# Kernel tuning notes

Measured on AMD Instinct MI355X. Metric: run time of the kernel, lower is better.

The kernel has to match this reference:

```python
import jax, jax.numpy as jnp
import numpy as np

WS = 7      # window size
SHIFT = 3   # shift size
NH = 6      # num heads
C = 192     # channels
HH = 56
WW = 56
B = 32


def _rel_coords():
    ch, cw = np.meshgrid(np.arange(WS), np.arange(WS), indexing='ij')
    coords = np.stack([ch, cw]).reshape(2, -1)            # (2, 49)
    rel = coords[:, :, None] - coords[:, None, :]          # (2, 49, 49)
    rel[0] += WS - 1
    rel[1] += WS - 1
    rel[0] *= 2 * WS - 1
    return rel.sum(0)                                      # (49, 49)


def _swin_attn_mask(Hp, Wp):
    img = np.zeros((Hp, Wp), np.int32)
    cnt = 0
    for hs in (slice(0, -WS), slice(-WS, -SHIFT), slice(-SHIFT, None)):
        for ws_ in (slice(0, -WS), slice(-WS, -SHIFT), slice(-SHIFT, None)):
            img[hs, ws_] = cnt
            cnt += 1
    win = img.reshape(Hp // WS, WS, Wp // WS, WS).transpose(0, 2, 1, 3).reshape(-1, WS * WS)
    return win[:, :, None] != win[:, None, :]              # (Nw, 49, 49) bool


def setup_inputs() -> dict:
    key = jax.random.key(0)
    ks = jax.random.split(key, 8)
    s = 0.02
    return {
        'x': jax.random.normal(ks[0], (B, HH * WW, C), jnp.float32),
        'H': HH,
        'W': WW,
        'attn_mask': jnp.asarray(_swin_attn_mask(HH, WW)),
        'relative_coords': jnp.asarray(_rel_coords(), jnp.int32),
        'norm1_w': jnp.ones((C,), jnp.float32),
        'norm1_b': jnp.zeros((C,), jnp.float32),
        'qkv_w': jax.random.normal(ks[1], (3 * C, C), jnp.float32) * s,
        'rel_bias': jax.random.normal(ks[2], ((2 * WS - 1) ** 2, NH), jnp.float32) * 0.2,
        'proj_w': jax.random.normal(ks[3], (C, C), jnp.float32) * s,
        'proj_b': jnp.zeros((C,), jnp.float32),
        'norm2_w': jnp.ones((C,), jnp.float32),
        'norm2_b': jnp.zeros((C,), jnp.float32),
        'fc1_w': jax.random.normal(ks[4], (4 * C, C), jnp.float32) * s,
        'fc1_b': jnp.zeros((4 * C,), jnp.float32),
        'fc2_w': jax.random.normal(ks[5], (C, 4 * C), jnp.float32) * s,
        'fc2_b': jnp.zeros((C,), jnp.float32),
    }


def _ln(t, w, b):
    m = t.mean(-1, keepdims=True)
    v = t.var(-1, keepdims=True)
    return (t - m) / jnp.sqrt(v + 1e-5) * w + b


def reference(x, H, W, attn_mask, relative_coords, norm1_w, norm1_b, qkv_w, rel_bias,
              proj_w, proj_b, norm2_w, norm2_b, fc1_w, fc1_b, fc2_w, fc2_b):
    Bb, L, Cd = x.shape
    nh, hd = NH, C // NH
    shortcut = x
    h = _ln(x, norm1_w, norm1_b).reshape(Bb, H, W, Cd)
    pad_h = (WS - H % WS) % WS
    pad_w = (WS - W % WS) % WS
    if pad_h or pad_w:
        h = jnp.pad(h, ((0, 0), (0, pad_h), (0, pad_w), (0, 0)))
    Hp, Wp = H + pad_h, W + pad_w
    if SHIFT > 0:
        h = jnp.roll(h, (-SHIFT, -SHIFT), axis=(1, 2))
    nWh, nWw = Hp // WS, Wp // WS
    Lw = WS * WS
    win = h.reshape(Bb, nWh, WS, nWw, WS, Cd).transpose(0, 1, 3, 2, 4, 5).reshape(-1, Lw, Cd)
    B_ = win.shape[0]
    qkv = (win @ qkv_w.T).reshape(B_, Lw, 3, nh, hd).transpose(2, 0, 3, 1, 4)
    q, k, v = qkv[0], qkv[1], qkv[2]
    # NOTE: source multiplies by num_dim**0.5 (faithful quirk)
    attn = jnp.einsum('bhid,bhjd->bhij', q, k) * (Cd ** 0.5)
    bias = rel_bias[relative_coords].transpose(2, 0, 1)    # (nh, Lw, Lw)
    attn = attn + bias[None]
    if SHIFT > 0:
        Nw = attn_mask.shape[0]
        attn = attn.reshape(-1, Nw, nh, Lw, Lw)
        attn = jnp.where(attn_mask[None, :, None], -100.0, attn)
        attn = attn.reshape(B_, nh, Lw, Lw)
    attn = jax.nn.softmax(attn, axis=-1)
    out = jnp.einsum('bhij,bhjd->bhid', attn, v).transpose(0, 2, 1, 3).reshape(B_, Lw, Cd)
    out = out @ proj_w.T + proj_b
    out = out.reshape(Bb, nWh, nWw, WS, WS, Cd).transpose(0, 1, 3, 2, 4, 5).reshape(Bb, Hp, Wp, Cd)
    if SHIFT > 0:
        out = jnp.roll(out, (SHIFT, SHIFT), axis=(1, 2))
    out = out[:, :H, :W].reshape(Bb, L, Cd)
    x = shortcut + out
    h2 = _ln(x, norm2_w, norm2_b)
    h2 = jax.nn.gelu(h2 @ fc1_w.T + fc1_b, approximate=False)
    # source MLP applies GELU (drop2 = act_layer()) after fc2 (faithful quirk)
    h2 = jax.nn.gelu(h2 @ fc2_w.T + fc2_b, approximate=False)
    return x + h2
```

## Files before the change

### kernel.cpp

```cpp
#include <hip/hip_runtime.h>

#define WS7    7
#define SHIFT3 3
#define NHEAD  6
#define CCH    192
#define HDIM   32
#define HH56   56
#define LTOK   (HH56*HH56)
#define NWIN   64
#define NBATCH 32
#define NWTOT  (NBATCH*NWIN)
#define LW     49
#define MTOK   (NWTOT*LW)

typedef unsigned short u16;
typedef unsigned int   u32;
typedef __bf16 b16;
typedef b16   b16x8 __attribute__((ext_vector_type(8)));
typedef u16   u16x8 __attribute__((ext_vector_type(8)));
typedef float f32x4 __attribute__((ext_vector_type(4)));

__device__ __forceinline__ float b2f(u16 u) {
    u32 x = ((u32)u) << 16;
    return __builtin_bit_cast(float, x);
}
__device__ __forceinline__ u16 f2b(float f) {
    u32 x = __builtin_bit_cast(u32, f);
    u32 r = x + 0x7FFFu + ((x >> 16) & 1u);
    return (u16)(r >> 16);
}
__device__ __forceinline__ float gelu_exact(float x) {
    return 0.5f * x * (1.0f + erff(x * 0.7071067811865475f));
}

__device__ __forceinline__ int map_token(int m, int &b) {
    int widx = m / LW, p = m - widx * LW;
    b = widx >> 6;
    int wloc = widx & 63;
    int wh = wloc >> 3, ww = wloc & 7;
    int i = p / WS7, j = p - i * WS7;
    int gh = wh * WS7 + i + SHIFT3; if (gh >= HH56) gh -= HH56;
    int gw = ww * WS7 + j + SHIFT3; if (gw >= HH56) gw -= HH56;
    return gh * HH56 + gw;
}

__global__ __launch_bounds__(1024) void probe_kernel(const u16* __restrict__ x, int* flag) {
    __shared__ int ch, cz;
    if (threadIdx.x == 0) { ch = 0; cz = 0; }
    __syncthreads();
    int i = threadIdx.x * 16;
    u16x8 a = *(const u16x8*)(x + i);
    u16x8 b = *(const u16x8*)(x + i + 8);
    int h = 0, z = 0;
    #pragma unroll
    for (int q = 0; q < 8; q++) {
        h += (((a[q] >> 7) & 0xFF) >= 0xC0) + (((b[q] >> 7) & 0xFF) >= 0xC0);
        z += (a[q] == 0) + (b[q] == 0);
    }
    #pragma unroll
    for (int off = 32; off > 0; off >>= 1) {
        h += __shfl_xor(h, off, 64);
        z += __shfl_xor(z, off, 64);
    }
    if ((threadIdx.x & 63) == 0) { atomicAdd(&ch, h); atomicAdd(&cz, z); }
    __syncthreads();
    if (threadIdx.x == 0) *flag = (ch > 250 || cz > 2048) ? 1 : 0;
}

#define CANON_TOTAL 445302
__global__ __launch_bounds__(256) void canon_all_kernel(
    const int* __restrict__ flag,
    const void* s0, const void* s1, const void* s2,  const void* s3,
    const void* s4, const void* s5, const void* s6,  const void* s7,
    const void* s8, const void* s9, const void* s10, const void* s11,
    char* __restrict__ ws)
{
    int i = blockIdx.x * 256 + threadIdx.x;
    if (i >= CANON_TOTAL) return;
    const void* srcs[12] = {s0, s1, s2, s3, s4, s5, s6, s7, s8, s9, s10, s11};
    const int cnt[12] = {110592, 36864, 147456, 147456, 192, 192, 192, 192, 192, 768, 192, 1014};
    const int off[12] = {64, 221248, 294976, 589888, 884800, 885184, 885568, 885952, 886336, 886720, 888256, 888640};
    int seg = 0, base = 0;
    while (seg < 11 && i >= base + cnt[seg]) { base += cnt[seg]; seg++; }
    int j = i - base;
    const void* sp = srcs[seg];
    u16* dp = (u16*)(ws + off[seg]);
    dp[j] = (*flag) ? f2b(((const float*)sp)[j]) : ((const u16*)sp)[j];
}

template<int GATHER>
__global__ __launch_bounds__(256) void ln_kernel(
    const void* __restrict__ src, const u16* __restrict__ w, const u16* __restrict__ bia,
    u16* __restrict__ dst, int m_base, const int* __restrict__ flag)
{
    int wave = threadIdx.x >> 6, lane = threadIdx.x & 63;
    int mloc = blockIdx.x * 4 + wave;
    size_t row;
    if (GATHER) { int b; int l = map_token(m_base + mloc, b); row = (size_t)b * LTOK + l; }
    else row = mloc;
    float v0, v1, v2;
    if (GATHER && *flag) {
        const float* xp = (const float*)src + row * CCH;
        v0 = xp[lane]; v1 = xp[lane + 64]; v2 = xp[lane + 128];
    } else {
        const u16* xp = (const u16*)src + row * CCH;
        v0 = b2f(xp[lane]); v1 = b2f(xp[lane + 64]); v2 = b2f(xp[lane + 128]);
    }
    float s = v0 + v1 + v2, sq = v0 * v0 + v1 * v1 + v2 * v2;
    for (int off = 32; off > 0; off >>= 1) {
        s  += __shfl_xor(s, off, 64);
        sq += __shfl_xor(sq, off, 64);
    }
    float mean = s * (1.f / 192.f);
    float var  = fmaxf(sq * (1.f / 192.f) - mean * mean, 0.f);
    float rstd = rsqrtf(var + 1e-5f);
    u16* op = dst + (size_t)mloc * CCH;
    op[lane]       = f2b((v0 - mean) * rstd * b2f(w[lane])       + b2f(bia[lane]));
    op[lane + 64]  = f2b((v1 - mean) * rstd * b2f(w[lane + 64])  + b2f(bia[lane + 64]));
    op[lane + 128] = f2b((v2 - mean) * rstd * b2f(w[lane + 128]) + b2f(bia[lane + 128]));
}

__device__ __forceinline__ void stage192(const u16* __restrict__ g, int ldg, u16* s, int tid) {
    #pragma unroll
    for (int it = 0; it < 7; it++) {
        int t = it * 256 + tid;
        if (t < 1600) {
            int row = t / 25, c = t - row * 25;
            int cc = (c == 24) ? 0 : c;
            const u16* src = g + (size_t)row * ldg + cc * 8;
            u16* dst = s + (size_t)(it * 256 + (tid & ~63)) * 8;
            __builtin_amdgcn_global_load_lds(
                (const __attribute__((address_space(1))) void*)src,
                (__attribute__((address_space(3))) void*)dst, 16, 0, 0);
        }
    }
}

__device__ __forceinline__ void ln_lds_rows(u16* As, const u16* __restrict__ w,
                                            const u16* __restrict__ bia, int tid) {
    int r = tid >> 2, p = tid & 3;
    u16* row = As + r * 200 + p * 48;
    u16x8 vv[6];
    float s = 0.f, sq = 0.f;
    #pragma unroll
    for (int j = 0; j < 6; j++) {
        vv[j] = *(const u16x8*)(row + j * 8);
        #pragma unroll
        for (int q = 0; q < 8; q++) { float f = b2f(vv[j][q]); s += f; sq += f * f; }
    }
    s  += __shfl_xor(s, 1, 64);  s  += __shfl_xor(s, 2, 64);
    sq += __shfl_xor(sq, 1, 64); sq += __shfl_xor(sq, 2, 64);
    float mean = s * (1.f / 192.f);
    float var  = fmaxf(sq * (1.f / 192.f) - mean * mean, 0.f);
    float rstd = rsqrtf(var + 1e-5f);
    #pragma unroll
    for (int j = 0; j < 6; j++) {
        u16x8 o;
        #pragma unroll
        for (int q = 0; q < 8; q++) {
            int col = p * 48 + j * 8 + q;
            o[q] = f2b((b2f(vv[j][q]) - mean) * rstd * b2f(w[col]) + b2f(bia[col]));
        }
        *(u16x8*)(row + j * 8) = o;
    }
}

template<int MODE, int NT, int LNF>
__global__ __launch_bounds__(256) void gemm_k192(
    const u16* __restrict__ A, const u16* __restrict__ Bm, int N,
    const u16* __restrict__ lnw, const u16* __restrict__ lnb,
    const u16* __restrict__ bias,
    u16* __restrict__ Cb, u16* __restrict__ X1, const void* __restrict__ Xin,
    int m_base, const int* __restrict__ flag)
{
    __shared__ __align__(16) u16 As[64 * 200];
    __shared__ __align__(16) u16 Bs[2][64 * 200];
    int isf = *flag;
    int tid = threadIdx.x;
    int m0 = blockIdx.x * 64;
    int wave = tid >> 6, lane = tid & 63;
    int wm = wave >> 1, wn = wave & 1;
    int quad = lane >> 4, mr = lane & 15;

    stage192(A + (size_t)m0 * 192, 192, As, tid);
    stage192(Bm, 192, Bs[0], tid);
    __syncthreads();
    if (LNF) { ln_lds_rows(As, lnw, lnb, tid); __syncthreads(); }

    const u16* pa0 = &As[(wm * 32 + mr) * 200 + quad * 8];
    #pragma unroll 1
    for (int nb = 0; nb < NT; nb++) {
        if (nb + 1 < NT)
            stage192(Bm + (size_t)(nb + 1) * 64 * 192, 192, Bs[(nb + 1) & 1], tid);
        const u16* pb0 = &Bs[nb & 1][(wn * 32 + mr) * 200 + quad * 8];
        f32x4 acc00 = {}, acc01 = {}, acc10 = {}, acc11 = {};
        #pragma unroll
        for (int ks = 0; ks < 6; ks++) {
            b16x8 a0 = __builtin_bit_cast(b16x8, *(const u16x8*)(pa0 + ks * 32));
            b16x8 a1 = __builtin_bit_cast(b16x8, *(const u16x8*)(pa0 + 16 * 200 + ks * 32));
            b16x8 b0 = __builtin_bit_cast(b16x8, *(const u16x8*)(pb0 + ks * 32));
            b16x8 b1 = __builtin_bit_cast(b16x8, *(const u16x8*)(pb0 + 16 * 200 + ks * 32));
            acc00 = __builtin_amdgcn_mfma_f32_16x16x32_bf16(a0, b0, acc00, 0, 0, 0);
            acc01 = __builtin_amdgcn_mfma_f32_16x16x32_bf16(a0, b1, acc01, 0, 0, 0);
            acc10 = __builtin_amdgcn_mfma_f32_16x16x32_bf16(a1, b0, acc10, 0, 0, 0);
            acc11 = __builtin_amdgcn_mfma_f32_16x16x32_bf16(a1, b1, acc11, 0, 0, 0);
        }
        int n0 = nb * 64;
        f32x4 accs[2][2] = {{acc00, acc01}, {acc10, acc11}};
        #pragma unroll
        for (int sm = 0; sm < 2; sm++) {
            #pragma unroll
            for (int sn = 0; sn < 2; sn++) {
                f32x4 v = accs[sm][sn];
                int nn = n0 + wn * 32 + sn * 16 + mr;
                int mb = m0 + wm * 32 + sm * 16 + quad * 4;
                #pragma unroll
                for (int r = 0; r < 4; r++) {
                    int mm = mb + r;
                    float val = v[r];
                    if (MODE == 0) {
                        Cb[(size_t)mm * N + nn] = f2b(val);
                    } else if (MODE == 1) {
                        val += b2f(bias[nn]);
                        int b; int l = map_token(m_base + mm, b);
                        size_t idx = ((size_t)b * LTOK + l) * CCH + nn;
                        float xi = isf ? ((const float*)Xin)[idx] : b2f(((const u16*)Xin)[idx]);
                        X1[idx] = f2b(xi + val);
                    } else {
                        val = gelu_exact(val + b2f(bias[nn]));
                        Cb[(size_t)mm * N + nn] = f2b(val);
                    }
                }
            }
        }
        __syncthreads();
    }
}

__global__ __launch_bounds__(256) void gemm_k768(
    const u16* __restrict__ A, const u16* __restrict__ Bm,
    const u16* __restrict__ bias, const u16* __restrict__ X1,
    void* __restrict__ Oout, size_t o_off, const int* __restrict__ flag)
{
    __shared__ __align__(16) u16 As[64 * 200];
    __shared__ __align__(16) u16 Bs[2][64 * 200];
    int isf = *flag;
    int tid = threadIdx.x;
    int m0 = blockIdx.x * 64;
    int wave = tid >> 6, lane = tid & 63;
    int wm = wave >> 1, wn = wave & 1;
    int quad = lane >> 4, mr = lane & 15;

    f32x4 acc[3][4] = {};

    const u16* pa0 = &As[(wm * 32 + mr) * 200 + quad * 8];
    #pragma unroll 1
    for (int k0 = 0; k0 < 768; k0 += 192) {
        stage192(A + (size_t)m0 * 768 + k0, 768, As, tid);
        stage192(Bm + k0, 768, Bs[0], tid);
        __syncthreads();
        #pragma unroll
        for (int nb = 0; nb < 3; nb++) {
            if (nb < 2)
                stage192(Bm + (size_t)(nb + 1) * 64 * 768 + k0, 768, Bs[(nb + 1) & 1], tid);
            const u16* pb0 = &Bs[nb & 1][(wn * 32 + mr) * 200 + quad * 8];
            #pragma unroll
            for (int ks = 0; ks < 6; ks++) {
                b16x8 a0 = __builtin_bit_cast(b16x8, *(const u16x8*)(pa0 + ks * 32));
                b16x8 a1 = __builtin_bit_cast(b16x8, *(const u16x8*)(pa0 + 16 * 200 + ks * 32));
                b16x8 b0 = __builtin_bit_cast(b16x8, *(const u16x8*)(pb0 + ks * 32));
                b16x8 b1 = __builtin_bit_cast(b16x8, *(const u16x8*)(pb0 + 16 * 200 + ks * 32));
                acc[nb][0] = __builtin_amdgcn_mfma_f32_16x16x32_bf16(a0, b0, acc[nb][0], 0, 0, 0);
                acc[nb][1] = __builtin_amdgcn_mfma_f32_16x16x32_bf16(a0, b1, acc[nb][1], 0, 0, 0);
                acc[nb][2] = __builtin_amdgcn_mfma_f32_16x16x32_bf16(a1, b0, acc[nb][2], 0, 0, 0);
                acc[nb][3] = __builtin_amdgcn_mfma_f32_16x16x32_bf16(a1, b1, acc[nb][3], 0, 0, 0);
            }
            __syncthreads();
        }
    }

    #pragma unroll
    for (int nb = 0; nb < 3; nb++) {
        #pragma unroll
        for (int sm = 0; sm < 2; sm++) {
            #pragma unroll
            for (int sn = 0; sn < 2; sn++) {
                f32x4 v = acc[nb][sm * 2 + sn];
                int nn = nb * 64 + wn * 32 + sn * 16 + mr;
                int mb = m0 + wm * 32 + sm * 16 + quad * 4;
                #pragma unroll
                for (int r = 0; r < 4; r++) {
                    int mm = mb + r;
                    float val = gelu_exact(v[r] + b2f(bias[nn]));
                    size_t idx = (size_t)mm * CCH + nn;
                    float r2 = val + b2f(X1[idx]);
                    if (isf) ((float*)Oout)[o_off + idx] = r2;
                    else     ((u16*)Oout)[o_off + idx]  = f2b(r2);
                }
            }
        }
    }
}

__global__ __launch_bounds__(256) void attn_kernel(
    const u16* __restrict__ qkv, const u16* __restrict__ rel_bias,
    u16* __restrict__ aout)
{
    __shared__ __align__(16) u16 qs[64 * 32];
    __shared__ __align__(16) u16 ks[64 * 32];
    __shared__ __align__(16) u16 vsT[32 * 72];
    __shared__ __align__(16) u16 ps[64 * 72];
    __shared__ float bias_s[169];
    int blk = blockIdx.x;
    int widx = blk / NHEAD, head = blk - widx * NHEAD;
    int wloc = widx & 63;
    int wh = wloc >> 3, ww = wloc & 7;
    int tid = threadIdx.x;
    const u16* base = qkv + (size_t)widx * LW * 576 + head * HDIM;

    if (tid < 196) {
        int i = tid >> 2, c8 = (tid & 3) * 8;
        *(uint4*)&qs[i * 32 + c8] = *(const uint4*)(base + (size_t)i * 576 + c8);
        *(uint4*)&ks[i * 32 + c8] = *(const uint4*)(base + (size_t)i * 576 + 192 + c8);
        u16x8 vv = *(const u16x8*)(base + (size_t)i * 576 + 384 + c8);
        #pragma unroll
        for (int q = 0; q < 8; q++) vsT[(c8 + q) * 72 + i] = vv[q];
    }
    for (int idx = tid; idx < 32 * 15; idx += 256) {
        int d = idx / 15, j = 49 + (idx - d * 15);
        vsT[d * 72 + j] = 0;
    }
    if (tid < 169) bias_s[tid] = b2f(rel_bias[tid * NHEAD + head]);
    __syncthreads();

    int wave = tid >> 6, lane = tid & 63;
    int quad = lane >> 4, c = lane & 15;

    b16x8 aq = __builtin_bit_cast(b16x8, *(const u16x8*)&qs[(wave * 16 + c) * 32 + quad * 8]);
    f32x4 sacc[4];
    #pragma unroll
    for (int nt = 0; nt < 4; nt++) {
        b16x8 bk = __builtin_bit_cast(b16x8, *(const u16x8*)&ks[(nt * 16 + c) * 32 + quad * 8]);
        f32x4 z = {};
        sacc[nt] = __builtin_amdgcn_mfma_f32_16x16x32_bf16(aq, bk, z, 0, 0, 0);
    }

    const float SCALE = 13.856406460551018f;
    float val[4][4];
    int rbase = wave * 16 + quad * 4;
    #pragma unroll
    for (int r = 0; r < 4; r++) {
        int i = rbase + r;
        int ih = i / WS7, iw = i - ih * WS7;
        int ri = (wh == 7 ? (ih < 4 ? 1 : 2) : 0) * 3 + (ww == 7 ? (iw < 4 ? 1 : 2) : 0);
        #pragma unroll
        for (int nt = 0; nt < 4; nt++) {
            int j = nt * 16 + c;
            float v;
            if (i >= LW) v = 0.f;
            else if (j >= LW) v = -1e30f;
            else {
                int jh = j / WS7, jw = j - jh * WS7;
                int rj = (wh == 7 ? (jh < 4 ? 1 : 2) : 0) * 3 + (ww == 7 ? (jw < 4 ? 1 : 2) : 0);
                if (ri != rj) v = -100.0f;
                else v = fmaf(sacc[nt][r], SCALE, bias_s[(ih - jh + 6) * 13 + (iw - jw + 6)]);
            }
            val[r][nt] = v;
        }
    }

    #pragma unroll
    for (int r = 0; r < 4; r++) {
        float mx = fmaxf(fmaxf(val[r][0], val[r][1]), fmaxf(val[r][2], val[r][3]));
        for (int d = 1; d < 16; d <<= 1) mx = fmaxf(mx, __shfl_xor(mx, d, 64));
        float sum = 0.f;
        #pragma unroll
        for (int nt = 0; nt < 4; nt++) { float e = expf(val[r][nt] - mx); val[r][nt] = e; sum += e; }
        for (int d = 1; d < 16; d <<= 1) sum += __shfl_xor(sum, d, 64);
        float inv = 1.f / sum;
        int i = rbase + r;
        #pragma unroll
        for (int nt = 0; nt < 4; nt++)
            ps[i * 72 + nt * 16 + c] = f2b(val[r][nt] * inv);
    }

    f32x4 oacc[2] = {{}, {}};
    #pragma unroll
    for (int kh = 0; kh < 2; kh++) {
        b16x8 ap = __builtin_bit_cast(b16x8, *(const u16x8*)&ps[(wave * 16 + c) * 72 + kh * 32 + quad * 8]);
        #pragma unroll
        for (int nt = 0; nt < 2; nt++) {
            b16x8 bv = __builtin_bit_cast(b16x8, *(const u16x8*)&vsT[(nt * 16 + c) * 72 + kh * 32 + quad * 8]);
            oacc[nt] = __builtin_amdgcn_mfma_f32_16x16x32_bf16(ap, bv, oacc[nt], 0, 0, 0);
        }
    }
    #pragma unroll
    for (int nt = 0; nt < 2; nt++) {
        #pragma unroll
        for (int r = 0; r < 4; r++) {
            int i = rbase + r;
            if (i < LW)
                aout[((size_t)widx * LW + i) * CCH + head * HDIM + nt * 16 + c] = f2b(oacc[nt][r]);
        }
    }
}

extern "C" void kernel_launch(void* const* d_in, const int* in_sizes, int n_in,
                              void* d_out, int out_size, void* d_ws, size_t ws_size,
                              hipStream_t stream)
{
    const void* x_in = d_in[0];
    char* ws = (char*)d_ws;
    int* flag = (int*)ws;

    u16* qkvw_c  = (u16*)(ws + 64);
    u16* projw_c = (u16*)(ws + 221248);
    u16* fc1w_c  = (u16*)(ws + 294976);
    u16* fc2w_c  = (u16*)(ws + 589888);
    u16* n1w_c   = (u16*)(ws + 884800);
    u16* n1b_c   = (u16*)(ws + 885184);
    u16* n2w_c   = (u16*)(ws + 885568);
    u16* n2b_c   = (u16*)(ws + 885952);
    u16* projb_c = (u16*)(ws + 886336);
    u16* fc1b_c  = (u16*)(ws + 886720);
    u16* fc2b_c  = (u16*)(ws + 888256);
    u16* relb_c  = (u16*)(ws + 888640);

    const size_t P0 = 1u << 20;
    const size_t X1SZ   = (size_t)MTOK * CCH * 2;
    const size_t QKVSZ  = (size_t)MTOK * 576 * 2;
    const size_t H1FULL = (size_t)MTOK * 768 * 2;

    u16* x1 = (u16*)(ws + P0);

    probe_kernel<<<1, 1024, 0, stream>>>((const u16*)x_in, flag);
    canon_all_kernel<<<(CANON_TOTAL + 255) / 256, 256, 0, stream>>>(
        flag,
        d_in[7], d_in[9], d_in[13], d_in[15],
        d_in[5], d_in[6], d_in[11], d_in[12],
        d_in[10], d_in[14], d_in[16], d_in[8],
        ws);

    int QC, EC;
    u16 *winq, *qkvq, *h1q;
    if (ws_size >= P0 + 2 * X1SZ + H1FULL) {
        QC = 1; EC = 1;
        winq = (u16*)(ws + P0 + X1SZ);
        qkvq = (u16*)(ws + P0 + 2 * X1SZ);
        h1q  = qkvq;
    } else if (ws_size >= P0 + 2 * X1SZ + QKVSZ) {
        QC = 1; EC = 2;
        winq = (u16*)(ws + P0 + X1SZ);
        qkvq = (u16*)(ws + P0 + 2 * X1SZ);
        h1q  = qkvq;
    } else {
        QC = 4; EC = 8;
        winq = (u16*)(ws + P0 + X1SZ);
        qkvq = (u16*)(ws + P0 + X1SZ + 9633792);
        h1q  = (u16*)(ws + P0 + X1SZ);
    }

    const int MQ = MTOK / QC;
    const int ME = MTOK / EC;

    for (int q = 0; q < QC; q++) {
        int mb = q * MQ;
        ln_kernel<1><<<MQ / 4, 256, 0, stream>>>(x_in, n1w_c, n1b_c, winq, mb, flag);
        gemm_k192<0, 9, 0><<<MQ / 64, 256, 0, stream>>>(
            winq, qkvw_c, 576, nullptr, nullptr, nullptr, qkvq, nullptr, nullptr, 0, flag);
        attn_kernel<<<(NWTOT / QC) * NHEAD, 256, 0, stream>>>(qkvq, relb_c, winq);
        gemm_k192<1, 3, 0><<<MQ / 64, 256, 0, stream>>>(
            winq, projw_c, 192, nullptr, nullptr, projb_c, nullptr, x1, x_in, mb, flag);
    }

    for (int e = 0; e < EC; e++) {
        size_t off = (size_t)e * ME * CCH;
        gemm_k192<2, 12, 1><<<ME / 64, 256, 0, stream>>>(
            x1 + off, fc1w_c, 768, n2w_c, n2b_c, fc1b_c, h1q, nullptr, nullptr, 0, flag);
        gemm_k768<<<ME / 64, 256, 0, stream>>>(
            h1q, fc2w_c, fc2b_c, x1 + off, d_out, off, flag);
    }
}
```

Baseline: 587.2 us.

## Unify GEMMs into 64x192 tiles with B loaded directly from global memory

Replaces the separate K=192 and K=768 GEMM kernels with one templated kernel. Each block computes a 64x192 output tile, splitting N across a second grid dimension. A is double-buffered in LDS over K chunks, while B fragments are read straight from global memory into registers with a one-step prefetch, so B no longer goes through LDS. This gives more blocks for the QKV and FC1 GEMMs and more MFMAs per A load, but relies on cache hits for the repeated B reads, raises accumulator register pressure (12 accumulators per wave), and recomputes LayerNorm per N-block in FC1.

```diff
diff --git a/kernel.cpp b/kernel.cpp
--- a/kernel.cpp
+++ b/kernel.cpp
@@ -165,133 +165,86 @@
     }
 }
 
-template<int MODE, int NT, int LNF>
-__global__ __launch_bounds__(256) void gemm_k192(
-    const u16* __restrict__ A, const u16* __restrict__ Bm, int N,
+template<int MODE, int LNF>
+__global__ __launch_bounds__(256) void gemm_bd(
+    const u16* __restrict__ A, const u16* __restrict__ Bm, int K, int N,
     const u16* __restrict__ lnw, const u16* __restrict__ lnb,
     const u16* __restrict__ bias,
     u16* __restrict__ Cb, u16* __restrict__ X1, const void* __restrict__ Xin,
-    int m_base, const int* __restrict__ flag)
+    void* __restrict__ Oout, size_t o_off, int m_base,
+    const int* __restrict__ flag)
 {
-    __shared__ __align__(16) u16 As[64 * 200];
-    __shared__ __align__(16) u16 Bs[2][64 * 200];
+    __shared__ __align__(16) u16 As[2][64 * 200];
     int isf = *flag;
     int tid = threadIdx.x;
     int m0 = blockIdx.x * 64;
+    int n0 = blockIdx.y * 192;
     int wave = tid >> 6, lane = tid & 63;
     int wm = wave >> 1, wn = wave & 1;
     int quad = lane >> 4, mr = lane & 15;
 
-    stage192(A + (size_t)m0 * 192, 192, As, tid);
-    stage192(Bm, 192, Bs[0], tid);
+    stage192(A + (size_t)m0 * K, K, As[0], tid);
     __syncthreads();
-    if (LNF) { ln_lds_rows(As, lnw, lnb, tid); __syncthreads(); }
-
-    const u16* pa0 = &As[(wm * 32 + mr) * 200 + quad * 8];
+    if (LNF) { ln_lds_rows(As[0], lnw, lnb, tid); __syncthreads(); }
+
+    f32x4 acc[2][6] = {};
+    int nchunks = K / 192;
+
     #pragma unroll 1
-    for (int nb = 0; nb < NT; nb++) {
-        if (nb + 1 < NT)
-            stage192(Bm + (size_t)(nb + 1) * 64 * 192, 192, Bs[(nb + 1) & 1], tid);
-        const u16* pb0 = &Bs[nb & 1][(wn * 32 + mr) * 200 + quad * 8];
-        f32x4 acc00 = {}, acc01 = {}, acc10 = {}, acc11 = {};
+    for (int c = 0; c < nchunks; c++) {
+        if (c) __syncthreads();
+        if (c + 1 < nchunks)
+            stage192(A + (size_t)m0 * K + (c + 1) * 192, K, As[(c + 1) & 1], tid);
+        const u16* pa = &As[c & 1][(wm * 32 + mr) * 200 + quad * 8];
+        const u16* gb = Bm + (size_t)(n0 + wn * 96 + mr) * K + (size_t)c * 192 + quad * 8;
+        u16x8 bf[6];
+        #pragma unroll
+        for (int sn = 0; sn < 6; sn++) bf[sn] = *(const u16x8*)(gb + (size_t)sn * 16 * K);
         #pragma unroll
         for (int ks = 0; ks < 6; ks++) {
-            b16x8 a0 = __builtin_bit_cast(b16x8, *(const u16x8*)(pa0 + ks * 32));
-            b16x8 a1 = __builtin_bit_cast(b16x8, *(const u16x8*)(pa0 + 16 * 200 + ks * 32));
-            b16x8 b0 = __builtin_bit_cast(b16x8, *(const u16x8*)(pb0 + ks * 32));
-            b16x8 b1 = __builtin_bit_cast(b16x8, *(const u16x8*)(pb0 + 16 * 200 + ks * 32));
-            acc00 = __builtin_amdgcn_mfma_f32_16x16x32_bf16(a0, b0, acc00, 0, 0, 0);
-            acc01 = __builtin_amdgcn_mfma_f32_16x16x32_bf16(a0, b1, acc01, 0, 0, 0);
-            acc10 = __builtin_amdgcn_mfma_f32_16x16x32_bf16(a1, b0, acc10, 0, 0, 0);
-            acc11 = __builtin_amdgcn_mfma_f32_16x16x32_bf16(a1, b1, acc11, 0, 0, 0);
-        }
-        int n0 = nb * 64;
-        f32x4 accs[2][2] = {{acc00, acc01}, {acc10, acc11}};
-        #pragma unroll
-        for (int sm = 0; sm < 2; sm++) {
+            b16x8 a0 = __builtin_bit_cast(b16x8, *(const u16x8*)(pa + ks * 32));
+            b16x8 a1 = __builtin_bit_cast(b16x8, *(const u16x8*)(pa + 16 * 200 + ks * 32));
+            u16x8 bcur[6];
             #pragma unroll
-            for (int sn = 0; sn < 2; sn++) {
-                f32x4 v = accs[sm][sn];
-                int nn = n0 + wn * 32 + sn * 16 + mr;
-                int mb = m0 + wm * 32 + sm * 16 + quad * 4;
+            for (int sn = 0; sn < 6; sn++) bcur[sn] = bf[sn];
+            if (ks < 5) {
                 #pragma unroll
-                for (int r = 0; r < 4; r++) {
-                    int mm = mb + r;
-                    float val = v[r];
-                    if (MODE == 0) {
-                        Cb[(size_t)mm * N + nn] = f2b(val);
-                    } else if (MODE == 1) {
-                        val += b2f(bias[nn]);
-                        int b; int l = map_token(m_base + mm, b);
-                        size_t idx = ((size_t)b * LTOK + l) * CCH + nn;
-                        float xi = isf ? ((const float*)Xin)[idx] : b2f(((const u16*)Xin)[idx]);
-                        X1[idx] = f2b(xi + val);
-                    } else {
-                        val = gelu_exact(val + b2f(bias[nn]));
-                        Cb[(size_t)mm * N + nn] = f2b(val);
-                    }
-                }
+                for (int sn = 0; sn < 6; sn++)
+                    bf[sn] = *(const u16x8*)(gb + (size_t)sn * 16 * K + (ks + 1) * 32);
             }
-        }
-        __syncthreads();
-    }
-}
-
-__global__ __launch_bounds__(256) void gemm_k768(
-    const u16* __restrict__ A, const u16* __restrict__ Bm,
-    const u16* __restrict__ bias, const u16* __restrict__ X1,
-    void* __restrict__ Oout, size_t o_off, const int* __restrict__ flag)
-{
-    __shared__ __align__(16) u16 As[64 * 200];
-    __shared__ __align__(16) u16 Bs[2][64 * 200];
-    int isf = *flag;
-    int tid = threadIdx.x;
-    int m0 = blockIdx.x * 64;
-    int wave = tid >> 6, lane = tid & 63;
-    int wm = wave >> 1, wn = wave & 1;
-    int quad = lane >> 4, mr = lane & 15;
-
-    f32x4 acc[3][4] = {};
-
-    const u16* pa0 = &As[(wm * 32 + mr) * 200 + quad * 8];
-    #pragma unroll 1
-    for (int k0 = 0; k0 < 768; k0 += 192) {
-        stage192(A + (size_t)m0 * 768 + k0, 768, As, tid);
-        stage192(Bm + k0, 768, Bs[0], tid);
-        __syncthreads();
-        #pragma unroll
-        for (int nb = 0; nb < 3; nb++) {
-            if (nb < 2)
-                stage192(Bm + (size_t)(nb + 1) * 64 * 768 + k0, 768, Bs[(nb + 1) & 1], tid);
-            const u16* pb0 = &Bs[nb & 1][(wn * 32 + mr) * 200 + quad * 8];
             #pragma unroll
-            for (int ks = 0; ks < 6; ks++) {
-                b16x8 a0 = __builtin_bit_cast(b16x8, *(const u16x8*)(pa0 + ks * 32));
-                b16x8 a1 = __builtin_bit_cast(b16x8, *(const u16x8*)(pa0 + 16 * 200 + ks * 32));
-                b16x8 b0 = __builtin_bit_cast(b16x8, *(const u16x8*)(pb0 + ks * 32));
-                b16x8 b1 = __builtin_bit_cast(b16x8, *(const u16x8*)(pb0 + 16 * 200 + ks * 32));
-                acc[nb][0] = __builtin_amdgcn_mfma_f32_16x16x32_bf16(a0, b0, acc[nb][0], 0, 0, 0);
-                acc[nb][1] = __builtin_amdgcn_mfma_f32_16x16x32_bf16(a0, b1, acc[nb][1], 0, 0, 0);
-                acc[nb][2] = __builtin_amdgcn_mfma_f32_16x16x32_bf16(a1, b0, acc[nb][2], 0, 0, 0);
-                acc[nb][3] = __builtin_amdgcn_mfma_f32_16x16x32_bf16(a1, b1, acc[nb][3], 0, 0, 0);
+            for (int sn = 0; sn < 6; sn++) {
+                b16x8 bb = __builtin_bit_cast(b16x8, bcur[sn]);
+                acc[0][sn] = __builtin_amdgcn_mfma_f32_16x16x32_bf16(a0, bb, acc[0][sn], 0, 0, 0);
+                acc[1][sn] = __builtin_amdgcn_mfma_f32_16x16x32_bf16(a1, bb, acc[1][sn], 0, 0, 0);
             }
-            __syncthreads();
-        }
-    }
-
-    #pragma unroll
-    for (int nb = 0; nb < 3; nb++) {
-        #pragma unroll
-        for (int sm = 0; sm < 2; sm++) {
+        }
+    }
+
+    #pragma unroll
+    for (int sm = 0; sm < 2; sm++) {
+        #pragma unroll
+        for (int sn = 0; sn < 6; sn++) {
+            f32x4 v = acc[sm][sn];
+            int nn = n0 + wn * 96 + sn * 16 + mr;
+            int mb = m0 + wm * 32 + sm * 16 + quad * 4;
             #pragma unroll
-            for (int sn = 0; sn < 2; sn++) {
-                f32x4 v = acc[nb][sm * 2 + sn];
-                int nn = nb * 64 + wn * 32 + sn * 16 + mr;
-                int mb = m0 + wm * 32 + sm * 16 + quad * 4;
-                #pragma unroll
-                for (int r = 0; r < 4; r++) {
-                    int mm = mb + r;
-                    float val = gelu_exact(v[r] + b2f(bias[nn]));
+            for (int r = 0; r < 4; r++) {
+                int mm = mb + r;
+                float val = v[r];
+                if (MODE == 0) {
+                    Cb[(size_t)mm * N + nn] = f2b(val);
+                } else if (MODE == 1) {
+                    val += b2f(bias[nn]);
+                    int b; int l = map_token(m_base + mm, b);
+                    size_t idx = ((size_t)b * LTOK + l) * CCH + nn;
+                    float xi = isf ? ((const float*)Xin)[idx] : b2f(((const u16*)Xin)[idx]);
+                    X1[idx] = f2b(xi + val);
+                } else if (MODE == 2) {
+                    val = gelu_exact(val + b2f(bias[nn]));
+                    Cb[(size_t)mm * N + nn] = f2b(val);
+                } else {
+                    val = gelu_exact(val + b2f(bias[nn]));
                     size_t idx = (size_t)mm * CCH + nn;
                     float r2 = val + b2f(X1[idx]);
                     if (isf) ((float*)Oout)[o_off + idx] = r2;
@@ -466,18 +419,22 @@
     for (int q = 0; q < QC; q++) {
         int mb = q * MQ;
         ln_kernel<1><<<MQ / 4, 256, 0, stream>>>(x_in, n1w_c, n1b_c, winq, mb, flag);
-        gemm_k192<0, 9, 0><<<MQ / 64, 256, 0, stream>>>(
-            winq, qkvw_c, 576, nullptr, nullptr, nullptr, qkvq, nullptr, nullptr, 0, flag);
+        gemm_bd<0, 0><<<dim3(MQ / 64, 3), 256, 0, stream>>>(
+            winq, qkvw_c, 192, 576, nullptr, nullptr, nullptr,
+            qkvq, nullptr, nullptr, nullptr, 0, 0, flag);
         attn_kernel<<<(NWTOT / QC) * NHEAD, 256, 0, stream>>>(qkvq, relb_c, winq);
-        gemm_k192<1, 3, 0><<<MQ / 64, 256, 0, stream>>>(
-            winq, projw_c, 192, nullptr, nullptr, projb_c, nullptr, x1, x_in, mb, flag);
+        gemm_bd<1, 0><<<dim3(MQ / 64, 1), 256, 0, stream>>>(
+            winq, projw_c, 192, 192, nullptr, nullptr, projb_c,
+            nullptr, x1, x_in, nullptr, 0, mb, flag);
     }
 
     for (int e = 0; e < EC; e++) {
         size_t off = (size_t)e * ME * CCH;
-        gemm_k192<2, 12, 1><<<ME / 64, 256, 0, stream>>>(
-            x1 + off, fc1w_c, 768, n2w_c, n2b_c, fc1b_c, h1q, nullptr, nullptr, 0, flag);
-        gemm_k768<<<ME / 64, 256, 0, stream>>>(
-            h1q, fc2w_c, fc2b_c, x1 + off, d_out, off, flag);
-    }
-}
+        gemm_bd<2, 1><<<dim3(ME / 64, 4), 256, 0, stream>>>(
+            x1 + off, fc1w_c, 192, 768, n2w_c, n2b_c, fc1b_c,
+            h1q, nullptr, nullptr, nullptr, 0, 0, flag);
+        gemm_bd<3, 0><<<dim3(ME / 64, 1), 256, 0, stream>>>(
+            h1q, fc2w_c, 768, 192, nullptr, nullptr, fc2b_c,
+            nullptr, x1 + off, nullptr, d_out, off, 0, flag);
+    }
+}
```

Measured after the change: 804.4 us. 37.0% more time.
